# Kernel optimization log

Hardware: AMD Instinct MI355X
Metric: run time of the kernel (lower is better)

The kernel has to match this reference:

```python
import jax, jax.numpy as jnp
import numpy as np

N_STEPS = 5
DT = 0.1
# radius fixed from initial sigma = 0.5 + 4.5*sigmoid(0.5) = 3.301 -> ceil(3*sigma) = 10
RADIUS = 10
SIZE = 2 * RADIUS + 1


def _pad1(x):
    return jnp.pad(x, ((0, 0), (0, 0), (1, 1), (1, 1)), mode='reflect')


def _spatial_gradient(x):
    p = _pad1(x)
    gy = (p[:, :, 2:, 1:-1] - p[:, :, :-2, 1:-1]) / 2.0
    gx = (p[:, :, 1:-1, 2:] - p[:, :, 1:-1, :-2]) / 2.0
    return gy, gx


def _laplacian(x):
    p = _pad1(x)
    return (p[:, :, :-2, 1:-1] + p[:, :, 2:, 1:-1]
            + p[:, :, 1:-1, :-2] + p[:, :, 1:-1, 2:] - 4.0 * x)


def _gaussian_blur(x, sigma):
    # differentiable kernel weights, fixed size (matches torch: radius from detached sigma)
    coords = jnp.arange(SIZE, dtype=x.dtype) - RADIUS
    k = jnp.exp(-coords ** 2 / (2.0 * sigma ** 2 + 1e-8))
    k = k / (k.sum() + 1e-8)
    xp = jnp.pad(x, ((0, 0), (0, 0), (0, 0), (RADIUS, RADIUS)), mode='reflect')
    out = jax.lax.conv_general_dilated(xp, k.reshape(1, 1, 1, SIZE), (1, 1), 'VALID')
    out = jnp.pad(out, ((0, 0), (0, 0), (RADIUS, RADIUS), (0, 0)), mode='reflect')
    out = jax.lax.conv_general_dilated(out, k.reshape(1, 1, SIZE, 1), (1, 1), 'VALID')
    return out


def _forward(image, lfd_map, alpha_raw, lambda_raw, log_sigma, log_beta, log_xi,
             eta_raw, nu_raw, log_gamma, omega_raw):
    sig = jax.nn.sigmoid
    alpha = 0.6 + 1.4 * sig(alpha_raw)
    lam = 0.01 + 0.19 * sig(lambda_raw)
    sigma = 0.5 + 4.5 * sig(log_sigma)
    beta = 1.0 + 4.0 * sig(log_beta)
    xi = 1.0 + 4.0 * sig(log_xi)
    eta = sig(eta_raw)
    nu = sig(nu_raw)
    gamma = 1.0 + 3.0 * sig(log_gamma)
    omega = sig(omega_raw)

    fractal_weight = jnp.clip(1.0 - omega * lfd_map, 0.0, 1.0)  # (B,1,H,W)
    u = image
    u0 = image
    for _ in range(N_STEPS):
        u_sigma = _gaussian_blur(u, sigma)
        gy, gx = _spatial_gradient(u)
        gys, gxs = _spatial_gradient(u_sigma)
        grad_mag = jnp.sqrt(gx ** 2 + gy ** 2 + 1e-8)
        grad_mag_s = jnp.sqrt(gxs ** 2 + gys ** 2 + 1e-8)
        lap_abs = jnp.abs(_laplacian(u))
        # conductance phi(s) = beta*sqrt(xi/(eta*s^2+eps)), clamped at 10
        phi = jnp.minimum(beta * jnp.sqrt(xi / (eta * grad_mag_s ** 2 + 1e-6)), 10.0)
        phi_f = phi * fractal_weight
        # curvature modulation psi'(s) = 1e-4*sqrt(nu*s^3+gamma), s = |grad u|*|lap u|
        s = grad_mag * lap_abs
        psi = 1e-4 * jnp.sqrt(nu * s ** 3 + gamma)
        pu = _pad1(u)
        dn = pu[:, :, :-2, 1:-1] - u
        dso = pu[:, :, 2:, 1:-1] - u
        de = pu[:, :, 1:-1, 2:] - u
        dw = pu[:, :, 1:-1, :-2] - u
        pp = _pad1(phi_f)
        div = (pp[:, :, :-2, 1:-1] * dn + pp[:, :, 2:, 1:-1] * dso
               + pp[:, :, 1:-1, 2:] * de + pp[:, :, 1:-1, :-2] * dw)
        du = alpha * psi * div - lam * (u - u0)
        u = jnp.clip(u + DT * du, 0.0, 1.0)
    edge_residual = jnp.abs(image - u)
    er_max = edge_residual.max(axis=(-2, -1), keepdims=True)
    edge_residual = edge_residual / (er_max + 1e-8)
    return u, edge_residual


def setup_inputs() -> dict:
    key = jax.random.key(0)
    k1, k2 = jax.random.split(key)
    B, H, W = 16, 512, 512
    image = jax.random.uniform(k1, (B, 1, H, W), jnp.float32)
    lfd_map = jax.random.uniform(k2, (B, 1, H, W), jnp.float32)
    f = lambda v: jnp.asarray(v, jnp.float32)
    return {
        'image': image, 'lfd_map': lfd_map,
        'alpha_raw': f(0.0), 'lambda_raw': f(-2.0), 'log_sigma': f(0.5),
        'log_beta': f(0.5), 'log_xi': f(0.5), 'eta_raw': f(0.3),
        'nu_raw': f(0.0), 'log_gamma': f(0.5), 'omega_raw': f(0.5),
    }


def reference(image, lfd_map, alpha_raw, lambda_raw, log_sigma, log_beta, log_xi,
              eta_raw, nu_raw, log_gamma, omega_raw):
    return _forward(image, lfd_map, alpha_raw, lambda_raw, log_sigma, log_beta,
                    log_xi, eta_raw, nu_raw, log_gamma, omega_raw)
```

## Files before the change

### kernel.cpp

```cpp
#include <hip/hip_runtime.h>
#include <math.h>

#define HH 512
#define WW 512
#define NPIX (16*HH*WW)
#define RAD 10
#define KS 21
#define TX 64
#define TY 32
#define SH 42
#define SW 74
#define SSTR 90

__device__ __forceinline__ int refl(int v, int n){ v = v < 0 ? -v : v; return v >= n ? 2*n - 2 - v : v; }
__device__ __forceinline__ float sigm(float x){ return 1.f/(1.f+expf(-x)); }

#define PARAMS_PRELUDE \
    const float alpha = 0.6f + 1.4f*sigm(a_raw[0]); \
    const float lam   = 0.01f + 0.19f*sigm(l_raw[0]); \
    const float beta  = 1.f + 4.f*sigm(lbeta[0]); \
    const float xi    = 1.f + 4.f*sigm(lxi[0]); \
    const float eta   = sigm(e_raw[0]); \
    const float nu    = sigm(n_raw[0]); \
    const float gam   = 1.f + 3.f*sigm(lgam[0]); \
    const float omg   = sigm(o_raw[0]); \
    const bool  sat   = (beta*beta*xi >= 100.f*(eta*0.5000002f + 1e-6f));

#define ROW6(v, S, off) float v##0=(S)[(off)], v##1=(S)[(off)+1], v##2=(S)[(off)+2], \
                              v##3=(S)[(off)+3], v##4=(S)[(off)+4], v##5=(S)[(off)+5];
#define ROW8S(v, S, off) float v##m=(S)[(off)-2], v##0=(S)[(off)], v##1=(S)[(off)+1], v##2=(S)[(off)+2], \
                               v##3=(S)[(off)+3], v##4=(S)[(off)+4], v##5=(S)[(off)+5], v##6=(S)[(off)+7];

__global__ __launch_bounds__(256) __attribute__((amdgpu_waves_per_eu(5)))
void k_mega(const float* __restrict__ img, const float* __restrict__ lfd,
            float* __restrict__ out_u, float* __restrict__ slots,
            const float* a_raw, const float* l_raw, const float* lbeta,
            const float* lxi, const float* e_raw, const float* n_raw,
            const float* lgam, const float* o_raw)
{
    PARAMS_PRELUDE
    if (!sat) return;
    __shared__ float SA[SH*SSTR];
    __shared__ float SB[SH*SSTR];
    __shared__ float red[4];
    const int tid = threadIdx.x;
    const bool active = tid < 240;
    const int py = tid / 12;
    const int px = tid - 12*py;
    const int ox = blockIdx.x * TX, oy = blockIdx.y * TY;
    const int b = blockIdx.z;
    const float* ib = img + (b<<18);
    const float* lb = lfd + (b<<18);
    const float A = 1e-3f*alpha;
    const float nuA = A*A*nu, gamA = A*A*gam;
    const bool bord = (ox == 0) | (oy == 0) | (ox == WW - TX) | (oy == HH - TY);

    for (int i = tid; i < SW*SH; i += 256){
        int r = i / SW, c = i - r*SW;
        int gy = oy - 5 + r, gx = ox - 5 + c;
        if (bord){ gy = refl(gy, HH); gx = refl(gx, WW); }
        int gi = gy*WW + gx;
        int pc = (c == 0) ? 0 : (c + (c-1)/6 + 1);
        SA[r*SSTR + pc] = ib[gi];
        SB[r*SSTR + pc] = fminf(fmaxf(1.f - omg*lb[gi], 0.f), 1.f);
    }
    __syncthreads();

    const int c0 = 1 + 6*px;
    const int r0 = 1 + 2*py;
    const int bi = r0*SSTR + 7*px + 2;

    ROW6(fa, SB, bi-SSTR) ROW8S(fb, SB, bi) ROW8S(fc, SB, bi+SSTR) ROW6(fd, SB, bi+2*SSTR)
    ROW6(zb, SA, bi) ROW6(zc, SA, bi+SSTR)
    __syncthreads();

    float ub0=zb0, ub1=zb1, ub2=zb2, ub3=zb3, ub4=zb4, ub5=zb5;
    float uc0=zc0, uc1=zc1, uc2=zc2, uc3=zc3, uc4=zc4, uc5=zc5;

    auto CF = [&](float cc, float cn, float cs, float cw, float ce,
                  float fn, float fs, float fw_, float fe, float z) -> float {
        float dy = cs - cn, dx = ce - cw;
        float g2 = fmaf(0.25f, fmaf(dy, dy, dx*dx), 1e-8f);
        float t1 = (cn + cs) + (ce + cw);
        float lap = fmaf(-4.f, cc, t1);
        float s = sqrtf(g2) * fabsf(lap);
        float psiA = sqrtf(fmaf(nuA, s*s*s, gamA));
        float dv = fn*(cn-cc) + fs*(cs-cc) + fe*(ce-cc) + fw_*(cw-cc);
        float du = fmaf(psiA, dv, -lam*(cc - z));
        return fminf(fmaxf(fmaf(0.1f, du, cc), 0.f), 1.f);
    };

#define READ_HALO(S) \
    ROW6(ua, S, bi-SSTR) ROW6(ud, S, bi+2*SSTR) \
    float ubm=(S)[bi-2], ub6=(S)[bi+7], ucm=(S)[bi+SSTR-2], uc6=(S)[bi+SSTR+7];

#define CELLS \
    float nb0 = CF(ub0, ua0, uc0, ubm, ub1, fa0, fc0, fbm, fb1, zb0); \
    float nb1 = CF(ub1, ua1, uc1, ub0, ub2, fa1, fc1, fb0, fb2, zb1); \
    float nb2 = CF(ub2, ua2, uc2, ub1, ub3, fa2, fc2, fb1, fb3, zb2); \
    float nb3 = CF(ub3, ua3, uc3, ub2, ub4, fa3, fc3, fb2, fb4, zb3); \
    float nb4 = CF(ub4, ua4, uc4, ub3, ub5, fa4, fc4, fb3, fb5, zb4); \
    float nb5 = CF(ub5, ua5, uc5, ub4, ub6, fa5, fc5, fb4, fb6, zb5); \
    float nc0 = CF(uc0, ub0, ud0, ucm, uc1, fb0, fd0, fcm, fc1, zc0); \
    float nc1 = CF(uc1, ub1, ud1, uc0, uc2, fb1, fd1, fc0, fc2, zc1); \
    float nc2 = CF(uc2, ub2, ud2, uc1, uc3, fb2, fd2, fc1, fc3, zc2); \
    float nc3 = CF(uc3, ub3, ud3, uc2, uc4, fb3, fd3, fc2, fc4, zc3); \
    float nc4 = CF(uc4, ub4, ud4, uc3, uc5, fb4, fd4, fc3, fc5, zc4); \
    float nc5 = CF(uc5, ub5, ud5, uc4, uc6, fb5, fd5, fc4, fc6, zc5);

#define STEP(S, D) { \
    READ_HALO(S) \
    CELLS \
    if (active){ \
        D[bi]   = nb0; D[bi+1] = nb1; D[bi+2] = nb2; D[bi+3] = nb3; D[bi+4] = nb4; D[bi+5] = nb5; \
        D[bi+SSTR]   = nc0; D[bi+SSTR+1] = nc1; D[bi+SSTR+2] = nc2; \
        D[bi+SSTR+3] = nc3; D[bi+SSTR+4] = nc4; D[bi+SSTR+5] = nc5; \
    } \
    ub0=nb0; ub1=nb1; ub2=nb2; ub3=nb3; ub4=nb4; ub5=nb5; \
    uc0=nc0; uc1=nc1; uc2=nc2; uc3=nc3; uc4=nc4; uc5=nc5; \
    } __syncthreads();

    STEP(SA, SB)
    STEP(SB, SA)
    STEP(SA, SB)
    STEP(SB, SA)

    float mymax = 0.f;
    {
        READ_HALO(SA)
        CELLS
        if (active && py >= 2 && py <= 17){
            float* ou = out_u + (b<<18) + (oy + r0 - 5)*WW + (ox + c0 - 5);
#define EMIT(K, NB, NC, ZB, ZC) \
            if (c0 + K >= 5 && c0 + K <= 68){ \
                ou[K] = NB; ou[WW + K] = NC; \
                mymax = fmaxf(mymax, fmaxf(fabsf(ZB - NB), fabsf(ZC - NC))); \
            }
            EMIT(0, nb0, nc0, zb0, zc0)
            EMIT(1, nb1, nc1, zb1, zc1)
            EMIT(2, nb2, nc2, zb2, zc2)
            EMIT(3, nb3, nc3, zb3, zc3)
            EMIT(4, nb4, nc4, zb4, zc4)
            EMIT(5, nb5, nc5, zb5, zc5)
#undef EMIT
        }
    }
#undef STEP
#undef CELLS
#undef READ_HALO

#pragma unroll
    for (int off = 32; off; off >>= 1) mymax = fmaxf(mymax, __shfl_down(mymax, off));
    if ((tid & 63) == 0) red[tid >> 6] = mymax;
    __syncthreads();
    if (tid == 0){
        float m = fmaxf(fmaxf(red[0], red[1]), fmaxf(red[2], red[3]));
        slots[(b<<7) + blockIdx.y*8 + blockIdx.x] = m;
    }
}

__global__ __launch_bounds__(256)
void k_iter(const float* __restrict__ src, const float* __restrict__ img,
            const float* __restrict__ lfd, float* __restrict__ dst,
            float* __restrict__ slots, int do_max,
            const float* a_raw, const float* l_raw, const float* lsig,
            const float* lbeta, const float* lxi, const float* e_raw,
            const float* n_raw, const float* lgam, const float* o_raw)
{
    PARAMS_PRELUDE
    if (sat) return;
    const float sigma = 0.5f + 4.5f*sigm(lsig[0]);
    float kw[KS];
    {
        float s = 0.f;
#pragma unroll
        for (int i = 0; i < KS; ++i){
            float c = (float)(i - RAD);
            kw[i] = expf(-c*c/(2.f*sigma*sigma + 1e-8f));
            s += kw[i];
        }
        float inv = 1.f/(s + 1e-8f);
#pragma unroll
        for (int i = 0; i < KS; ++i) kw[i] *= inv;
    }

    __shared__ __attribute__((aligned(16))) float sh[56][72];
    __shared__ float su[36][72];
    __shared__ float ut[34][72];
    __shared__ float red[4];
    float (*pt)[72] = sh;

    const int tid = threadIdx.x;
    const int x0 = blockIdx.x * TX;
    const int y0 = blockIdx.y * TY;
    const int b  = blockIdx.z;
    const float* sb = src + (b << 18);
    const float* ib = img + (b << 18);
    const float* lb = lfd + (b << 18);
    float* db = dst + (b << 18);

#pragma unroll
    for (int p = 0; p < 9; ++p) {
        int i = tid + p * 256;
        if (i < 34 * 66) {
            int r = i / 66, c = i - r * 66;
            ut[r][c] = sb[refl(y0 - 1 + r, HH) * WW + refl(x0 - 1 + c, WW)];
        }
    }
#pragma unroll
    for (int p = 0; p < 4; ++p) {
        int i = tid + p * 256;
        if (i < 56 * 17) {
            int hr = i / 17, g = i - hr * 17;
            const float* row = sb + refl(y0 - 12 + hr, HH) * WW;
            int gxs = x0 - 12 + 4 * g;
            float wv[24];
            if (gxs >= 0 && gxs + 23 < WW) {
                const float4* p4 = (const float4*)(row + gxs);
#pragma unroll
                for (int q = 0; q < 6; ++q) {
                    float4 v = p4[q];
                    wv[4*q] = v.x; wv[4*q+1] = v.y; wv[4*q+2] = v.z; wv[4*q+3] = v.w;
                }
            } else {
#pragma unroll
                for (int q = 0; q < 24; ++q) wv[q] = row[refl(gxs + q, WW)];
            }
            float a0 = 0.f, a1 = 0.f, a2 = 0.f, a3 = 0.f;
#pragma unroll
            for (int j = 0; j < KS; ++j) {
                a0 = fmaf(kw[j], wv[j],     a0);
                a1 = fmaf(kw[j], wv[j + 1], a1);
                a2 = fmaf(kw[j], wv[j + 2], a2);
                a3 = fmaf(kw[j], wv[j + 3], a3);
            }
            float4 o; o.x = a0; o.y = a1; o.z = a2; o.w = a3;
            *(float4*)&sh[hr][4 * g] = o;
        }
    }
    __syncthreads();
#pragma unroll
    for (int p = 0; p < 3; ++p) {
        int i = tid + p * 256;
        if (i < 9 * 68) {
            int rg = i / 68, c = i - rg * 68;
            int r0 = rg * 4;
            float a0 = 0.f, a1 = 0.f, a2 = 0.f, a3 = 0.f;
#pragma unroll
            for (int q = 0; q < 24; ++q) {
                float s = sh[r0 + q][c];
                if (q <= 20)           a0 = fmaf(kw[q],     s, a0);
                if (q >= 1 && q <= 21) a1 = fmaf(kw[q - 1], s, a1);
                if (q >= 2 && q <= 22) a2 = fmaf(kw[q - 2], s, a2);
                if (q >= 3)            a3 = fmaf(kw[q - 3], s, a3);
            }
            su[r0][c] = a0; su[r0+1][c] = a1; su[r0+2][c] = a2; su[r0+3][c] = a3;
        }
    }
    __syncthreads();
#pragma unroll
    for (int p = 0; p < 9; ++p) {
        int i = tid + p * 256;
        if (i < 34 * 66) {
            int r = i / 66, c = i - r * 66;
            float gys = (su[r + 2][c + 1] - su[r][c + 1]) * 0.5f;
            float gxs = (su[r + 1][c + 2] - su[r + 1][c]) * 0.5f;
            float g2 = fmaf(gxs, gxs, fmaf(gys, gys, 1e-8f));
            float ph = fminf(beta * sqrtf(xi / fmaf(eta, g2, 1e-6f)), 10.f);
            float lv = lb[refl(y0 - 1 + r, HH) * WW + refl(x0 - 1 + c, WW)];
            float fwv = fminf(fmaxf(1.f - omg * lv, 0.f), 1.f);
            pt[r][c] = ph * fwv;
        }
    }
    __syncthreads();
    const int c = tid & 63, r0 = tid >> 6;
    float mymax = 0.f;
#pragma unroll
    for (int p = 0; p < 8; ++p) {
        int r = r0 + p * 4;
        float uc = ut[r + 1][c + 1];
        float uN = ut[r][c + 1],     uS = ut[r + 2][c + 1];
        float uE = ut[r + 1][c + 2], uW = ut[r + 1][c];
        float gy = (uS - uN) * 0.5f, gx = (uE - uW) * 0.5f;
        float lap = uN + uS + uE + uW - 4.f * uc;
        float gm = sqrtf(fmaf(gx, gx, fmaf(gy, gy, 1e-8f)));
        float s = gm * fabsf(lap);
        float psi = 1e-4f * sqrtf(fmaf(nu, s * s * s, gam));
        float pN = pt[r][c + 1],     pS = pt[r + 2][c + 1];
        float pE = pt[r + 1][c + 2], pW = pt[r + 1][c];
        float dv = pN * (uN - uc) + pS * (uS - uc) + pE * (uE - uc) + pW * (uW - uc);
        int gidx = (y0 + r) * WW + x0 + c;
        float u0v = ib[gidx];
        float du = alpha * psi * dv - lam * (uc - u0v);
        float un = fminf(fmaxf(fmaf(0.1f, du, uc), 0.f), 1.f);
        db[gidx] = un;
        mymax = fmaxf(mymax, fabsf(u0v - un));
    }
    if (do_max) {
#pragma unroll
        for (int off = 32; off; off >>= 1) mymax = fmaxf(mymax, __shfl_down(mymax, off));
        if ((tid & 63) == 0) red[tid >> 6] = mymax;
        __syncthreads();
        if (tid == 0) {
            float m = fmaxf(fmaxf(red[0], red[1]), fmaxf(red[2], red[3]));
            slots[(b << 7) + blockIdx.y*8 + blockIdx.x] = m;
        }
    }
}

__global__ __launch_bounds__(256)
void k_res2(const float* __restrict__ img, const float* __restrict__ u,
            float* __restrict__ r, const float* __restrict__ slots)
{
    __shared__ float sm[2];
    const int tid = threadIdx.x;
    const int blk = blockIdx.x;
    const int b = blk >> 6;
    float m = 0.f;
    if (tid < 128) m = slots[(b << 7) + tid];
#pragma unroll
    for (int off = 32; off; off >>= 1) m = fmaxf(m, __shfl_down(m, off));
    if (tid == 0)  sm[0] = m;
    if (tid == 64) sm[1] = m;
    __syncthreads();
    const float inv = 1.f / (fmaxf(sm[0], sm[1]) + 1e-8f);
    const int base = blk * 1024 + tid;
#pragma unroll
    for (int k = 0; k < 4; ++k){
        int i = base + k * 256;
        float4 a = ((const float4*)img)[i];
        float4 c = ((const float4*)u)[i];
        float4 o;
        o.x = fabsf(a.x - c.x) * inv;
        o.y = fabsf(a.y - c.y) * inv;
        o.z = fabsf(a.z - c.z) * inv;
        o.w = fabsf(a.w - c.w) * inv;
        ((float4*)r)[i] = o;
    }
}

extern "C" void kernel_launch(void* const* d_in, const int* in_sizes, int n_in,
                              void* d_out, int out_size, void* d_ws, size_t ws_size,
                              hipStream_t stream)
{
    const float* image = (const float*)d_in[0];
    const float* lfd   = (const float*)d_in[1];
    const float* a_raw = (const float*)d_in[2];
    const float* l_raw = (const float*)d_in[3];
    const float* lsig  = (const float*)d_in[4];
    const float* lbeta = (const float*)d_in[5];
    const float* lxi   = (const float*)d_in[6];
    const float* e_raw = (const float*)d_in[7];
    const float* n_raw = (const float*)d_in[8];
    const float* lgam  = (const float*)d_in[9];
    const float* o_raw = (const float*)d_in[10];

    float* out_u = (float*)d_out;
    float* out_r = out_u + NPIX;

    float* uB    = (float*)d_ws;
    float* slots = uB + NPIX;

    dim3 grd(WW/TX, HH/TY, 16), blk(256);

    k_mega<<<grd, blk, 0, stream>>>(image, lfd, out_u, slots,
                                    a_raw, l_raw, lbeta, lxi, e_raw, n_raw, lgam, o_raw);

    float* bufs[2] = { out_u, uB };
    for (int it = 0; it < 5; ++it) {
        const float* src = (it == 0) ? image : bufs[(it + 1) & 1];
        float* dstp = bufs[it & 1];
        k_iter<<<grd, blk, 0, stream>>>(src, image, lfd, dstp, slots, it == 4 ? 1 : 0,
                                        a_raw, l_raw, lsig, lbeta, lxi, e_raw, n_raw, lgam, o_raw);
    }

    k_res2<<<1024, 256, 0, stream>>>(image, out_u, out_r, slots);
}
```

Measured before the change: 81.06 us.

## Use single shared buffer in mega kernel to cut LDS and raise occupancy

Replaces the double-buffered SA/SB shared arrays with one buffer. The fractal weights and the image are now staged through it in two passes, and each step adds an extra barrier so that all halo reads finish before the in-place writes. It also drops the waves_per_eu hint and computes only the needed parameters after the early-return check. The aim is to halve LDS per block so more blocks fit per CU, at the cost of more barriers per step and a serialized load phase.

New measurement: 87.93 us. +8.5%, slower.

```diff
diff --git a/kernel.cpp b/kernel.cpp
--- a/kernel.cpp
+++ b/kernel.cpp
@@ -15,15 +15,10 @@
 __device__ __forceinline__ int refl(int v, int n){ v = v < 0 ? -v : v; return v >= n ? 2*n - 2 - v : v; }
 __device__ __forceinline__ float sigm(float x){ return 1.f/(1.f+expf(-x)); }
 
-#define PARAMS_PRELUDE \
-    const float alpha = 0.6f + 1.4f*sigm(a_raw[0]); \
-    const float lam   = 0.01f + 0.19f*sigm(l_raw[0]); \
+#define SAT_CHECK \
     const float beta  = 1.f + 4.f*sigm(lbeta[0]); \
     const float xi    = 1.f + 4.f*sigm(lxi[0]); \
     const float eta   = sigm(e_raw[0]); \
-    const float nu    = sigm(n_raw[0]); \
-    const float gam   = 1.f + 3.f*sigm(lgam[0]); \
-    const float omg   = sigm(o_raw[0]); \
     const bool  sat   = (beta*beta*xi >= 100.f*(eta*0.5000002f + 1e-6f));
 
 #define ROW6(v, S, off) float v##0=(S)[(off)], v##1=(S)[(off)+1], v##2=(S)[(off)+2], \
@@ -31,22 +26,28 @@
 #define ROW8S(v, S, off) float v##m=(S)[(off)-2], v##0=(S)[(off)], v##1=(S)[(off)+1], v##2=(S)[(off)+2], \
                                v##3=(S)[(off)+3], v##4=(S)[(off)+4], v##5=(S)[(off)+5], v##6=(S)[(off)+7];
 
-__global__ __launch_bounds__(256) __attribute__((amdgpu_waves_per_eu(5)))
+__global__ __launch_bounds__(256)
 void k_mega(const float* __restrict__ img, const float* __restrict__ lfd,
             float* __restrict__ out_u, float* __restrict__ slots,
             const float* a_raw, const float* l_raw, const float* lbeta,
             const float* lxi, const float* e_raw, const float* n_raw,
             const float* lgam, const float* o_raw)
 {
-    PARAMS_PRELUDE
+    SAT_CHECK
     if (!sat) return;
-    __shared__ float SA[SH*SSTR];
-    __shared__ float SB[SH*SSTR];
+    const float alpha = 0.6f + 1.4f*sigm(a_raw[0]);
+    const float lam   = 0.01f + 0.19f*sigm(l_raw[0]);
+    const float nu    = sigm(n_raw[0]);
+    const float gam   = 1.f + 3.f*sigm(lgam[0]);
+    const float omg   = sigm(o_raw[0]);
+
+    __shared__ float S[SH*SSTR];
     __shared__ float red[4];
     const int tid = threadIdx.x;
     const bool active = tid < 240;
-    const int py = tid / 12;
-    const int px = tid - 12*py;
+    const int pid = (tid < 240) ? tid : 239;
+    const int py = pid / 12;
+    const int px = pid - 12*py;
     const int ox = blockIdx.x * TX, oy = blockIdx.y * TY;
     const int b = blockIdx.z;
     const float* ib = img + (b<<18);
@@ -55,24 +56,30 @@
     const float nuA = A*A*nu, gamA = A*A*gam;
     const bool bord = (ox == 0) | (oy == 0) | (ox == WW - TX) | (oy == HH - TY);
 
+    const int c0 = 1 + 6*px;
+    const int r0 = 1 + 2*py;
+    const int bi = r0*SSTR + 7*px + 2;
+
     for (int i = tid; i < SW*SH; i += 256){
         int r = i / SW, c = i - r*SW;
         int gy = oy - 5 + r, gx = ox - 5 + c;
         if (bord){ gy = refl(gy, HH); gx = refl(gx, WW); }
-        int gi = gy*WW + gx;
         int pc = (c == 0) ? 0 : (c + (c-1)/6 + 1);
-        SA[r*SSTR + pc] = ib[gi];
-        SB[r*SSTR + pc] = fminf(fmaxf(1.f - omg*lb[gi], 0.f), 1.f);
-    }
-    __syncthreads();
-
-    const int c0 = 1 + 6*px;
-    const int r0 = 1 + 2*py;
-    const int bi = r0*SSTR + 7*px + 2;
-
-    ROW6(fa, SB, bi-SSTR) ROW8S(fb, SB, bi) ROW8S(fc, SB, bi+SSTR) ROW6(fd, SB, bi+2*SSTR)
-    ROW6(zb, SA, bi) ROW6(zc, SA, bi+SSTR)
-    __syncthreads();
+        S[r*SSTR + pc] = fminf(fmaxf(1.f - omg*lb[gy*WW + gx], 0.f), 1.f);
+    }
+    __syncthreads();
+    ROW6(fa, S, bi-SSTR) ROW8S(fb, S, bi) ROW8S(fc, S, bi+SSTR) ROW6(fd, S, bi+2*SSTR)
+    __syncthreads();
+
+    for (int i = tid; i < SW*SH; i += 256){
+        int r = i / SW, c = i - r*SW;
+        int gy = oy - 5 + r, gx = ox - 5 + c;
+        if (bord){ gy = refl(gy, HH); gx = refl(gx, WW); }
+        int pc = (c == 0) ? 0 : (c + (c-1)/6 + 1);
+        S[r*SSTR + pc] = ib[gy*WW + gx];
+    }
+    __syncthreads();
+    ROW6(zb, S, bi) ROW6(zc, S, bi+SSTR)
 
     float ub0=zb0, ub1=zb1, ub2=zb2, ub3=zb3, ub4=zb4, ub5=zb5;
     float uc0=zc0, uc1=zc1, uc2=zc2, uc3=zc3, uc4=zc4, uc5=zc5;
@@ -90,9 +97,9 @@
         return fminf(fmaxf(fmaf(0.1f, du, cc), 0.f), 1.f);
     };
 
-#define READ_HALO(S) \
+#define READ_HALO \
     ROW6(ua, S, bi-SSTR) ROW6(ud, S, bi+2*SSTR) \
-    float ubm=(S)[bi-2], ub6=(S)[bi+7], ucm=(S)[bi+SSTR-2], uc6=(S)[bi+SSTR+7];
+    float ubm=S[bi-2], ub6=S[bi+7], ucm=S[bi+SSTR-2], uc6=S[bi+SSTR+7];
 
 #define CELLS \
     float nb0 = CF(ub0, ua0, uc0, ubm, ub1, fa0, fc0, fbm, fb1, zb0); \
@@ -108,26 +115,24 @@
     float nc4 = CF(uc4, ub4, ud4, uc3, uc5, fb4, fd4, fc3, fc5, zc4); \
     float nc5 = CF(uc5, ub5, ud5, uc4, uc6, fb5, fd5, fc4, fc6, zc5);
 
-#define STEP(S, D) { \
-    READ_HALO(S) \
-    CELLS \
-    if (active){ \
-        D[bi]   = nb0; D[bi+1] = nb1; D[bi+2] = nb2; D[bi+3] = nb3; D[bi+4] = nb4; D[bi+5] = nb5; \
-        D[bi+SSTR]   = nc0; D[bi+SSTR+1] = nc1; D[bi+SSTR+2] = nc2; \
-        D[bi+SSTR+3] = nc3; D[bi+SSTR+4] = nc4; D[bi+SSTR+5] = nc5; \
-    } \
-    ub0=nb0; ub1=nb1; ub2=nb2; ub3=nb3; ub4=nb4; ub5=nb5; \
-    uc0=nc0; uc1=nc1; uc2=nc2; uc3=nc3; uc4=nc4; uc5=nc5; \
-    } __syncthreads();
-
-    STEP(SA, SB)
-    STEP(SB, SA)
-    STEP(SA, SB)
-    STEP(SB, SA)
+#pragma unroll
+    for (int it = 0; it < 4; ++it){
+        READ_HALO
+        CELLS
+        __syncthreads();
+        if (active){
+            S[bi]   = nb0; S[bi+1] = nb1; S[bi+2] = nb2; S[bi+3] = nb3; S[bi+4] = nb4; S[bi+5] = nb5;
+            S[bi+SSTR]   = nc0; S[bi+SSTR+1] = nc1; S[bi+SSTR+2] = nc2;
+            S[bi+SSTR+3] = nc3; S[bi+SSTR+4] = nc4; S[bi+SSTR+5] = nc5;
+        }
+        ub0=nb0; ub1=nb1; ub2=nb2; ub3=nb3; ub4=nb4; ub5=nb5;
+        uc0=nc0; uc1=nc1; uc2=nc2; uc3=nc3; uc4=nc4; uc5=nc5;
+        __syncthreads();
+    }
 
     float mymax = 0.f;
     {
-        READ_HALO(SA)
+        READ_HALO
         CELLS
         if (active && py >= 2 && py <= 17){
             float* ou = out_u + (b<<18) + (oy + r0 - 5)*WW + (ox + c0 - 5);
@@ -145,7 +150,6 @@
 #undef EMIT
         }
     }
-#undef STEP
 #undef CELLS
 #undef READ_HALO
 
@@ -167,8 +171,13 @@
             const float* lbeta, const float* lxi, const float* e_raw,
             const float* n_raw, const float* lgam, const float* o_raw)
 {
-    PARAMS_PRELUDE
+    SAT_CHECK
     if (sat) return;
+    const float alpha = 0.6f + 1.4f*sigm(a_raw[0]);
+    const float lam   = 0.01f + 0.19f*sigm(l_raw[0]);
+    const float nu    = sigm(n_raw[0]);
+    const float gam   = 1.f + 3.f*sigm(lgam[0]);
+    const float omg   = sigm(o_raw[0]);
     const float sigma = 0.5f + 4.5f*sigm(lsig[0]);
     float kw[KS];
     {
```
